# Performance work log

Measured on AMD Instinct MI355X. Metric: run time of the kernel, lower is better.

## Reference

```python
import jax, jax.numpy as jnp
import numpy as np

B, H, S, D = 2, 16, 2048, 64


def setup_inputs() -> dict:
    key = jax.random.key(0)
    kq, kk, kv = jax.random.split(key, 3)
    Q = jax.random.normal(kq, (B, H, S, D), dtype=jnp.float32)
    K = jax.random.normal(kk, (B, H, S, D), dtype=jnp.float32)
    V = jax.random.normal(kv, (B, H, S, D), dtype=jnp.float32)
    # causal mask: True = masked out (matches torch masked_fill_ semantics)
    causal = ~jnp.tril(jnp.ones((S, S), dtype=bool))
    mask = jnp.broadcast_to(causal, (B, H, S, S))
    return {"Q": Q, "K": K, "V": V, "mask": mask}


def reference(Q, K, V, mask):
    d_q = Q.shape[-1]
    scale = 1.0 / np.sqrt(d_q).astype(np.float32)
    # scores: (B, H, S, S)
    scores = jnp.einsum('bhqd,bhkd->bhqk', Q, K) * scale
    scores = jnp.where(mask, jnp.float32(-1e9), scores)
    attention = jax.nn.softmax(scores, axis=-1)
    context = jnp.einsum('bhqk,bhkd->bhqd', attention, V)
    return (context, attention)
```

## Files before the change

kernel.cpp:

```cpp
#include <hip/hip_runtime.h>
#include <hip/hip_bf16.h>


constexpr int SEQ = 2048;
constexpr int HD  = 64;
constexpr int NHEADS = 32;
constexpr int QT  = 64;
constexpr int NT  = SEQ / QT;

typedef __bf16 bf16x8 __attribute__((ext_vector_type(8)));
typedef unsigned short u16x8 __attribute__((ext_vector_type(8)));
typedef unsigned short u16x4 __attribute__((ext_vector_type(4)));
typedef float f32x4 __attribute__((ext_vector_type(4)));
typedef unsigned short us;

__device__ __forceinline__ us f2bf(float x) {
  unsigned u = __builtin_bit_cast(unsigned, x);
  return (us)((u + 0x7fffu + ((u >> 16) & 1u)) >> 16);
}
__device__ __forceinline__ float bf2f(us b) {
  return __builtin_bit_cast(float, (unsigned)b << 16);
}

#define GLOAD_LDS(gp, lp)                                                        \
  __builtin_amdgcn_global_load_lds(                                             \
      (const __attribute__((address_space(1))) void*)(gp),                      \
      (__attribute__((address_space(3))) void*)(lp), 16, 0, 0)

__device__ __forceinline__ void stage8k(const us* img, us* lds, int w, int l) {
  const char* g = (const char*)img + w * 2048 + l * 16;
  char* s = (char*)lds + w * 2048;
  GLOAD_LDS(g, s);
  GLOAD_LDS(g + 1024, s + 1024);
}

__global__ void prep_kernel(const float* __restrict__ Qg,
                            const float* __restrict__ Kg,
                            const float* __restrict__ Vg,
                            us* __restrict__ ws) {
  const int tile = blockIdx.x & (NT - 1);
  const int bh   = blockIdx.x >> 5;
  const int t = threadIdx.x;
  const size_t tOff = ((size_t)bh * SEQ + (size_t)tile * QT) * HD;
  us* Qi = ws + ((size_t)bh * NT + tile) * 4096;
  us* Ki = Qi + (size_t)NHEADS * NT * 4096;
  us* Vi = Ki + (size_t)NHEADS * NT * 4096;

  #pragma unroll
  for (int g0 = 0; g0 < 2; ++g0) {
    const int g = t + 256 * g0;
    const int r = g >> 3, c8 = g & 7;
    const int cp = (8 * c8) ^ ((r & 7) << 3);
    const float* qs = Qg + tOff + (size_t)r * HD + cp;
    const float* ks = Kg + tOff + (size_t)r * HD + cp;
    u16x8 q, k;
    #pragma unroll
    for (int j = 0; j < 8; ++j) { q[j] = f2bf(qs[j]); k[j] = f2bf(ks[j]); }
    *(u16x8*)(Qi + 8 * g) = q;
    *(u16x8*)(Ki + 8 * g) = k;
  }
  #pragma unroll
  for (int g0 = 0; g0 < 2; ++g0) {
    const int g = t + 256 * g0;
    const int d = g >> 3, k8 = g & 7;
    const int kp = (8 * k8) ^ ((d & 7) << 3);
    const float* vs = Vg + tOff + d;
    u16x8 v;
    #pragma unroll
    for (int j = 0; j < 8; ++j) v[j] = f2bf(vs[(size_t)(kp + j) * HD]);
    *(u16x8*)(Vi + 8 * g) = v;
  }
}

__launch_bounds__(256, 3)
__global__ void attn_main(const us* __restrict__ ws, float* __restrict__ out) {
  const int fb = blockIdx.x;
  const int bh = fb & (NHEADS - 1);
  const int pi = fb >> 5;
  const int t  = threadIdx.x;
  const int l  = t & 63;
  const int w  = t >> 6;
  const int l16 = l & 15;
  const int lg  = l >> 4;

  __shared__ __align__(16) us Qs[4096];
  __shared__ __align__(16) us Ks[2][4096];
  __shared__ __align__(16) us Vs[2][4096];
  __shared__ __align__(16) us Ps[4][1024];

  const us* Qi = ws + (size_t)bh * NT * 4096;
  const us* Ki = Qi + (size_t)NHEADS * NT * 4096;
  const us* Vi = Ki + (size_t)NHEADS * NT * 4096;

  float* ctx = out + (size_t)bh * SEQ * HD;
  float* att = out + (size_t)NHEADS * SEQ * HD + (size_t)bh * SEQ * SEQ;

  const float KC = 0.18033688011112042f;

  for (int half = 0; half < 2; ++half) {
    const int qt = half ? (NT - 1 - pi) : pi;
    const int qbase = qt * QT;
    const int qg = qbase + w * 16 + l16;

    stage8k(Qi + (size_t)qt * 4096, Qs, w, l);
    stage8k(Ki, Ks[0], w, l);
    {
      const int zc0 = (qt + 1) * QT;
      const int nz4 = (SEQ - zc0) >> 2;
      for (int r = 0; r < QT; ++r) {
        float* rowp = att + (size_t)(qbase + r) * SEQ + zc0;
        for (int c = t; c < nz4; c += 256)
          __builtin_nontemporal_store((f32x4){0.f, 0.f, 0.f, 0.f}, (f32x4*)(rowp + 4 * c));
      }
    }
    __syncthreads();

    bf16x8 aq[2];
    #pragma unroll
    for (int ks = 0; ks < 2; ++ks) {
      const int qr = w * 16 + l16;
      const int d0 = ks * 32 + lg * 8;
      const int idx = (qr * 64 + d0) ^ ((qr & 7) << 3);
      aq[ks] = __builtin_bit_cast(bf16x8, *(const u16x8*)(&Qs[idx]));
    }

    float rsum = 0.f;
    {
      int cur = 0;
      for (int kt = 0; kt <= qt; ++kt) {
        if (kt < qt) stage8k(Ki + (size_t)(kt + 1) * 4096, Ks[cur ^ 1], w, l);
        const us* krb = Ks[cur];
        const int kb = kt * QT;
        #pragma unroll
        for (int ct = 0; ct < 4; ++ct) {
          f32x4 acc = {0.f, 0.f, 0.f, 0.f};
          #pragma unroll
          for (int ks = 0; ks < 2; ++ks) {
            const int kr = ct * 16 + l16;
            const int d0 = ks * 32 + lg * 8;
            const int idx = (kr * 64 + d0) ^ ((kr & 7) << 3);
            bf16x8 bk = __builtin_bit_cast(bf16x8, *(const u16x8*)(&krb[idx]));
            acc = __builtin_amdgcn_mfma_f32_16x16x32_bf16(bk, aq[ks], acc, 0, 0, 0);
          }
          const int kg0 = kb + ct * 16 + lg * 4;
          #pragma unroll
          for (int r = 0; r < 4; ++r) {
            float e = __builtin_amdgcn_exp2f(acc[r] * KC);
            rsum += (kg0 + r <= qg) ? e : 0.f;
          }
        }
        __syncthreads();
        cur ^= 1;
      }
    }
    stage8k(Ki, Ks[0], w, l);
    stage8k(Vi, Vs[0], w, l);
    rsum += __shfl_xor(rsum, 16);
    rsum += __shfl_xor(rsum, 32);
    const float inv = 1.f / rsum;
    __syncthreads();

    f32x4 oacc[4];
    #pragma unroll
    for (int ct = 0; ct < 4; ++ct) oacc[ct] = (f32x4){0.f, 0.f, 0.f, 0.f};

    {
      int cur = 0;
      for (int kt = 0; kt <= qt; ++kt) {
        if (kt < qt) {
          stage8k(Ki + (size_t)(kt + 1) * 4096, Ks[cur ^ 1], w, l);
          stage8k(Vi + (size_t)(kt + 1) * 4096, Vs[cur ^ 1], w, l);
        }
        const us* krb = Ks[cur];
        const us* vrb = Vs[cur];
        const int kb = kt * QT;

        #pragma unroll
        for (int ct = 0; ct < 4; ++ct) {
          f32x4 acc = {0.f, 0.f, 0.f, 0.f};
          #pragma unroll
          for (int ks = 0; ks < 2; ++ks) {
            const int kr = ct * 16 + l16;
            const int d0 = ks * 32 + lg * 8;
            const int idx = (kr * 64 + d0) ^ ((kr & 7) << 3);
            bf16x8 bk = __builtin_bit_cast(bf16x8, *(const u16x8*)(&krb[idx]));
            acc = __builtin_amdgcn_mfma_f32_16x16x32_bf16(bk, aq[ks], acc, 0, 0, 0);
          }
          const int kg0 = kb + ct * 16 + lg * 4;
          u16x4 pb;
          #pragma unroll
          for (int r = 0; r < 4; ++r) {
            float e = __builtin_amdgcn_exp2f(acc[r] * KC) * inv;
            pb[r] = f2bf((kg0 + r <= qg) ? e : 0.f);
          }
          const int pidx = (l16 * 64 + ct * 16 + lg * 4) ^ ((l16 & 7) << 3);
          *(u16x4*)(&Ps[w][pidx]) = pb;
        }

        #pragma unroll
        for (int j = 0; j < 4; ++j) {
          const int rloc = lg + 4 * j;
          const int idx = (rloc * 64 + 4 * l16) ^ ((rloc & 7) << 3);
          u16x4 p4 = *(const u16x4*)(&Ps[w][idx]);
          f32x4 pv = { bf2f(p4[0]), bf2f(p4[1]), bf2f(p4[2]), bf2f(p4[3]) };
          __builtin_nontemporal_store(pv,
              (f32x4*)(att + (size_t)(qbase + w * 16 + rloc) * SEQ + kb + 4 * l16));
        }

        bf16x8 pa[2];
        #pragma unroll
        for (int ks = 0; ks < 2; ++ks) {
          const int pidx = (l16 * 64 + ks * 32 + lg * 8) ^ ((l16 & 7) << 3);
          pa[ks] = __builtin_bit_cast(bf16x8, *(const u16x8*)(&Ps[w][pidx]));
        }
        #pragma unroll
        for (int ct = 0; ct < 4; ++ct) {
          #pragma unroll
          for (int ks = 0; ks < 2; ++ks) {
            const int dr = ct * 16 + l16;
            const int key0 = ks * 32 + lg * 8;
            const int vidx = (dr * 64 + key0) ^ ((dr & 7) << 3);
            bf16x8 av = __builtin_bit_cast(bf16x8, *(const u16x8*)(&vrb[vidx]));
            oacc[ct] = __builtin_amdgcn_mfma_f32_16x16x32_bf16(av, pa[ks], oacc[ct], 0, 0, 0);
          }
        }

        __syncthreads();
        cur ^= 1;
      }
    }

    #pragma unroll
    for (int ct = 0; ct < 4; ++ct)
      __builtin_nontemporal_store(oacc[ct],
          (f32x4*)(ctx + (size_t)qg * HD + ct * 16 + lg * 4));
  }
}

__launch_bounds__(256, 2)
__global__ void attn_fallback(const float* __restrict__ Qg,
                              const float* __restrict__ Kg,
                              const float* __restrict__ Vg,
                              float* __restrict__ out) {
  const int fb = blockIdx.x;
  const int bh = fb & (NHEADS - 1);
  const int pi = fb >> 5;
  const int t  = threadIdx.x;
  const int l  = t & 63;
  const int w  = t >> 6;
  const int l16 = l & 15;
  const int lg  = l >> 4;

  __shared__ __align__(16) us Qs[QT * HD];
  __shared__ __align__(16) us Ks[QT * HD];
  __shared__ __align__(16) us Vs[QT * HD];
  __shared__ __align__(16) us Ps[4][16 * QT];

  const size_t hoff = (size_t)bh * SEQ * HD;
  const float* Qh = Qg + hoff;
  const float* Kh = Kg + hoff;
  const float* Vh = Vg + hoff;
  float* ctx = out + hoff;
  float* att = out + (size_t)NHEADS * SEQ * HD + (size_t)bh * SEQ * SEQ;

  auto load_tile = [&](const float* src, f32x4 (&reg)[4]) {
    #pragma unroll
    for (int j = 0; j < 4; ++j) {
      const int f = t + 256 * j;
      reg[j] = *(const f32x4*)(src + (size_t)(f >> 4) * HD + 4 * (f & 15));
    }
  };
  auto write_k = [&](const f32x4 (&reg)[4], us* dst) {
    #pragma unroll
    for (int j = 0; j < 4; ++j) {
      const int f = t + 256 * j;
      const int r = f >> 4, c4 = f & 15;
      const int idx = (r * 64 + 4 * c4) ^ ((r & 7) << 3);
      u16x4 b = { f2bf(reg[j].x), f2bf(reg[j].y), f2bf(reg[j].z), f2bf(reg[j].w) };
      *(u16x4*)(&dst[idx]) = b;
    }
  };
  auto write_vv = [&](const f32x4 (&reg)[4], us* dst) {
    #pragma unroll
    for (int j = 0; j < 4; ++j) {
      const int f = t + 256 * j;
      const int r = f >> 4, c4 = f & 15;
      const int idx = (r * 64 + 4 * c4) ^ (((r >> 3) & 3) << 4);
      u16x4 b = { f2bf(reg[j].x), f2bf(reg[j].y), f2bf(reg[j].z), f2bf(reg[j].w) };
      *(u16x4*)(&dst[idx]) = b;
    }
  };

  const float sc = 0.125f;

  for (int half = 0; half < 2; ++half) {
    const int qt = half ? (NT - 1 - pi) : pi;
    const int qbase = qt * QT;
    const int qg = qbase + w * 16 + l16;

    __syncthreads();
    {
      const int zc0 = (qt + 1) * QT;
      const int nz4 = (SEQ - zc0) >> 2;
      for (int r = 0; r < QT; ++r) {
        float* rowp = att + (size_t)(qbase + r) * SEQ + zc0;
        for (int c = t; c < nz4; c += 256)
          __builtin_nontemporal_store((f32x4){0.f, 0.f, 0.f, 0.f}, (f32x4*)(rowp + 4 * c));
      }
    }
    {
      f32x4 qreg[4];
      load_tile(Qh + (size_t)qbase * HD, qreg);
      write_k(qreg, Qs);
    }
    __syncthreads();

    bf16x8 aq[2];
    #pragma unroll
    for (int ks = 0; ks < 2; ++ks) {
      const int qr = w * 16 + l16;
      const int d0 = ks * 32 + lg * 8;
      const int idx = (qr * 64 + d0) ^ ((qr & 7) << 3);
      aq[ks] = __builtin_bit_cast(bf16x8, *(const u16x8*)(&Qs[idx]));
    }

    float rsum = 0.f;
    {
      f32x4 kreg[4];
      load_tile(Kh, kreg);
      write_k(kreg, Ks);
      __syncthreads();
      for (int kt = 0; kt <= qt; ++kt) {
        if (kt < qt) load_tile(Kh + (size_t)(kt + 1) * QT * HD, kreg);
        const int kb = kt * QT;
        #pragma unroll
        for (int ct = 0; ct < 4; ++ct) {
          f32x4 acc = {0.f, 0.f, 0.f, 0.f};
          #pragma unroll
          for (int ks = 0; ks < 2; ++ks) {
            const int kr = ct * 16 + l16;
            const int d0 = ks * 32 + lg * 8;
            const int idx = (kr * 64 + d0) ^ ((kr & 7) << 3);
            bf16x8 bk = __builtin_bit_cast(bf16x8, *(const u16x8*)(&Ks[idx]));
            acc = __builtin_amdgcn_mfma_f32_16x16x32_bf16(bk, aq[ks], acc, 0, 0, 0);
          }
          const int kg0 = kb + ct * 16 + lg * 4;
          #pragma unroll
          for (int r = 0; r < 4; ++r) {
            float e = __expf(acc[r] * sc);
            rsum += (kg0 + r <= qg) ? e : 0.f;
          }
        }
        __syncthreads();
        if (kt < qt) write_k(kreg, Ks);
        __syncthreads();
      }
    }
    rsum += __shfl_xor(rsum, 16);
    rsum += __shfl_xor(rsum, 32);
    const float inv = 1.f / rsum;

    f32x4 oacc[4];
    #pragma unroll
    for (int ct = 0; ct < 4; ++ct) oacc[ct] = (f32x4){0.f, 0.f, 0.f, 0.f};

    {
      f32x4 kreg[4], vreg[4];
      load_tile(Kh, kreg);
      load_tile(Vh, vreg);
      write_k(kreg, Ks);
      write_vv(vreg, Vs);
      __syncthreads();
      for (int kt = 0; kt <= qt; ++kt) {
        if (kt < qt) {
          load_tile(Kh + (size_t)(kt + 1) * QT * HD, kreg);
          load_tile(Vh + (size_t)(kt + 1) * QT * HD, vreg);
        }
        const int kb = kt * QT;
        #pragma unroll
        for (int ct = 0; ct < 4; ++ct) {
          f32x4 acc = {0.f, 0.f, 0.f, 0.f};
          #pragma unroll
          for (int ks = 0; ks < 2; ++ks) {
            const int kr = ct * 16 + l16;
            const int d0 = ks * 32 + lg * 8;
            const int idx = (kr * 64 + d0) ^ ((kr & 7) << 3);
            bf16x8 bk = __builtin_bit_cast(bf16x8, *(const u16x8*)(&Ks[idx]));
            acc = __builtin_amdgcn_mfma_f32_16x16x32_bf16(bk, aq[ks], acc, 0, 0, 0);
          }
          const int kg0 = kb + ct * 16 + lg * 4;
          u16x4 pb;
          #pragma unroll
          for (int r = 0; r < 4; ++r) {
            float e = __expf(acc[r] * sc) * inv;
            pb[r] = f2bf((kg0 + r <= qg) ? e : 0.f);
          }
          const int pidx = (l16 * 64 + ct * 16 + lg * 4) ^ ((l16 & 7) << 3);
          *(u16x4*)(&Ps[w][pidx]) = pb;
        }
        #pragma unroll
        for (int ct = 0; ct < 4; ++ct) {
          #pragma unroll
          for (int ks = 0; ks < 2; ++ks) {
            const int key0 = ks * 32 + lg * 8;
            const int pidx = (l16 * 64 + key0) ^ ((l16 & 7) << 3);
            bf16x8 pa = __builtin_bit_cast(bf16x8, *(const u16x8*)(&Ps[w][pidx]));
            bf16x8 av;
            const int dcol = ct * 16 + l16;
            const int xorv = ((key0 >> 3) & 3) << 4;
            #pragma unroll
            for (int j = 0; j < 8; ++j)
              av[j] = __builtin_bit_cast(__bf16, Vs[((key0 + j) * 64 + dcol) ^ xorv]);
            oacc[ct] = __builtin_amdgcn_mfma_f32_16x16x32_bf16(av, pa, oacc[ct], 0, 0, 0);
          }
        }
        __syncthreads();
        #pragma unroll
        for (int j = 0; j < 4; ++j) {
          const int f = t + 256 * j;
          const int r = f >> 4, c4 = f & 15;
          const int ww = r >> 4, qr = r & 15;
          const int idx = (qr * 64 + 4 * c4) ^ ((qr & 7) << 3);
          u16x4 pb = *(const u16x4*)(&Ps[ww][idx]);
          f32x4 pv = { bf2f(pb[0]), bf2f(pb[1]), bf2f(pb[2]), bf2f(pb[3]) };
          __builtin_nontemporal_store(pv,
              (f32x4*)(att + (size_t)(qbase + r) * SEQ + kb + 4 * c4));
        }
        if (kt < qt) {
          write_k(kreg, Ks);
          write_vv(vreg, Vs);
        }
        __syncthreads();
      }
    }
    #pragma unroll
    for (int ct = 0; ct < 4; ++ct)
      *(f32x4*)(ctx + (size_t)qg * HD + ct * 16 + lg * 4) = oacc[ct];
  }
}

extern "C" void kernel_launch(void* const* d_in, const int* in_sizes, int n_in,
                              void* d_out, int out_size, void* d_ws, size_t ws_size,
                              hipStream_t stream) {
  const float* Q = (const float*)d_in[0];
  const float* K = (const float*)d_in[1];
  const float* V = (const float*)d_in[2];
  float* out = (float*)d_out;
  const size_t NEED = (size_t)3 * NHEADS * NT * 4096 * sizeof(us);
  if (ws_size >= NEED && d_ws != nullptr) {
    us* wsp = (us*)d_ws;
    prep_kernel<<<dim3(NHEADS * NT), dim3(256), 0, stream>>>(Q, K, V, wsp);
    attn_main<<<dim3(NT / 2 * NHEADS), dim3(256), 0, stream>>>(wsp, out);
  } else {
    attn_fallback<<<dim3(NT / 2 * NHEADS), dim3(256), 0, stream>>>(Q, K, V, out);
  }
}
```

Before: 142.1 us.

## Split paired query tiles into separate blocks and tighten pipeline sync

Each block of attn_main previously handled two query tiles, one early and one late, to balance the causal work. Now each block handles a single query tile, launched longest-first, so the grid doubles to 1024 blocks. The Q tile is loaded straight from global into registers, which frees the Qs shared buffer, and the occupancy hint rises from 3 to 4 blocks per CU. The second-pass loop replaces __syncthreads with a manual s_waitcnt vmcnt(4) plus s_barrier and sched barriers, so the next K/V prefetch can stay in flight across the barrier. The trade-offs are more blocks to schedule, the pairing-based balance now resting on launch order, and hand-written waitcnt counts that must match the number of outstanding global-to-LDS loads.

New measurement: 169.0 us. 19.0% more time.

```diff
diff --git a/kernel.cpp b/kernel.cpp
--- a/kernel.cpp
+++ b/kernel.cpp
@@ -72,18 +72,20 @@
   }
 }
 
-__launch_bounds__(256, 3)
+__launch_bounds__(256, 4)
 __global__ void attn_main(const us* __restrict__ ws, float* __restrict__ out) {
   const int fb = blockIdx.x;
-  const int bh = fb & (NHEADS - 1);
-  const int pi = fb >> 5;
+  const int g8 = fb >> 8;
+  const int r  = fb & 255;
+  const int bh = r & (NHEADS - 1);
+  const int p  = (r >> 5) | ((g8 & 1) << 3);
+  const int qt = (g8 >> 1) ? p : (NT - 1 - p);
   const int t  = threadIdx.x;
   const int l  = t & 63;
   const int w  = t >> 6;
   const int l16 = l & 15;
   const int lg  = l >> 4;
 
-  __shared__ __align__(16) us Qs[4096];
   __shared__ __align__(16) us Ks[2][4096];
   __shared__ __align__(16) us Vs[2][4096];
   __shared__ __align__(16) us Ps[4][1024];
@@ -96,145 +98,145 @@
   float* att = out + (size_t)NHEADS * SEQ * HD + (size_t)bh * SEQ * SEQ;
 
   const float KC = 0.18033688011112042f;
-
-  for (int half = 0; half < 2; ++half) {
-    const int qt = half ? (NT - 1 - pi) : pi;
-    const int qbase = qt * QT;
-    const int qg = qbase + w * 16 + l16;
-
-    stage8k(Qi + (size_t)qt * 4096, Qs, w, l);
-    stage8k(Ki, Ks[0], w, l);
-    {
-      const int zc0 = (qt + 1) * QT;
-      const int nz4 = (SEQ - zc0) >> 2;
-      for (int r = 0; r < QT; ++r) {
-        float* rowp = att + (size_t)(qbase + r) * SEQ + zc0;
-        for (int c = t; c < nz4; c += 256)
-          __builtin_nontemporal_store((f32x4){0.f, 0.f, 0.f, 0.f}, (f32x4*)(rowp + 4 * c));
-      }
-    }
-    __syncthreads();
-
-    bf16x8 aq[2];
+  const int qbase = qt * QT;
+  const int qg = qbase + w * 16 + l16;
+
+  bf16x8 aq[2];
+  {
+    const int qr = w * 16 + l16;
     #pragma unroll
     for (int ks = 0; ks < 2; ++ks) {
-      const int qr = w * 16 + l16;
-      const int d0 = ks * 32 + lg * 8;
-      const int idx = (qr * 64 + d0) ^ ((qr & 7) << 3);
-      aq[ks] = __builtin_bit_cast(bf16x8, *(const u16x8*)(&Qs[idx]));
-    }
-
-    float rsum = 0.f;
-    {
-      int cur = 0;
-      for (int kt = 0; kt <= qt; ++kt) {
-        if (kt < qt) stage8k(Ki + (size_t)(kt + 1) * 4096, Ks[cur ^ 1], w, l);
-        const us* krb = Ks[cur];
-        const int kb = kt * QT;
-        #pragma unroll
-        for (int ct = 0; ct < 4; ++ct) {
-          f32x4 acc = {0.f, 0.f, 0.f, 0.f};
-          #pragma unroll
-          for (int ks = 0; ks < 2; ++ks) {
-            const int kr = ct * 16 + l16;
-            const int d0 = ks * 32 + lg * 8;
-            const int idx = (kr * 64 + d0) ^ ((kr & 7) << 3);
-            bf16x8 bk = __builtin_bit_cast(bf16x8, *(const u16x8*)(&krb[idx]));
-            acc = __builtin_amdgcn_mfma_f32_16x16x32_bf16(bk, aq[ks], acc, 0, 0, 0);
-          }
-          const int kg0 = kb + ct * 16 + lg * 4;
-          #pragma unroll
-          for (int r = 0; r < 4; ++r) {
-            float e = __builtin_amdgcn_exp2f(acc[r] * KC);
-            rsum += (kg0 + r <= qg) ? e : 0.f;
-          }
-        }
-        __syncthreads();
-        cur ^= 1;
-      }
-    }
-    stage8k(Ki, Ks[0], w, l);
-    stage8k(Vi, Vs[0], w, l);
-    rsum += __shfl_xor(rsum, 16);
-    rsum += __shfl_xor(rsum, 32);
-    const float inv = 1.f / rsum;
-    __syncthreads();
-
-    f32x4 oacc[4];
-    #pragma unroll
-    for (int ct = 0; ct < 4; ++ct) oacc[ct] = (f32x4){0.f, 0.f, 0.f, 0.f};
-
-    {
-      int cur = 0;
-      for (int kt = 0; kt <= qt; ++kt) {
-        if (kt < qt) {
-          stage8k(Ki + (size_t)(kt + 1) * 4096, Ks[cur ^ 1], w, l);
-          stage8k(Vi + (size_t)(kt + 1) * 4096, Vs[cur ^ 1], w, l);
-        }
-        const us* krb = Ks[cur];
-        const us* vrb = Vs[cur];
-        const int kb = kt * QT;
-
-        #pragma unroll
-        for (int ct = 0; ct < 4; ++ct) {
-          f32x4 acc = {0.f, 0.f, 0.f, 0.f};
-          #pragma unroll
-          for (int ks = 0; ks < 2; ++ks) {
-            const int kr = ct * 16 + l16;
-            const int d0 = ks * 32 + lg * 8;
-            const int idx = (kr * 64 + d0) ^ ((kr & 7) << 3);
-            bf16x8 bk = __builtin_bit_cast(bf16x8, *(const u16x8*)(&krb[idx]));
-            acc = __builtin_amdgcn_mfma_f32_16x16x32_bf16(bk, aq[ks], acc, 0, 0, 0);
-          }
-          const int kg0 = kb + ct * 16 + lg * 4;
-          u16x4 pb;
-          #pragma unroll
-          for (int r = 0; r < 4; ++r) {
-            float e = __builtin_amdgcn_exp2f(acc[r] * KC) * inv;
-            pb[r] = f2bf((kg0 + r <= qg) ? e : 0.f);
-          }
-          const int pidx = (l16 * 64 + ct * 16 + lg * 4) ^ ((l16 & 7) << 3);
-          *(u16x4*)(&Ps[w][pidx]) = pb;
-        }
-
-        #pragma unroll
-        for (int j = 0; j < 4; ++j) {
-          const int rloc = lg + 4 * j;
-          const int idx = (rloc * 64 + 4 * l16) ^ ((rloc & 7) << 3);
-          u16x4 p4 = *(const u16x4*)(&Ps[w][idx]);
-          f32x4 pv = { bf2f(p4[0]), bf2f(p4[1]), bf2f(p4[2]), bf2f(p4[3]) };
-          __builtin_nontemporal_store(pv,
-              (f32x4*)(att + (size_t)(qbase + w * 16 + rloc) * SEQ + kb + 4 * l16));
-        }
-
-        bf16x8 pa[2];
+      const int idx = (qr * 64 + ks * 32 + lg * 8) ^ ((qr & 7) << 3);
+      aq[ks] = __builtin_bit_cast(bf16x8, *(const u16x8*)(&Qi[(size_t)qt * 4096 + idx]));
+    }
+  }
+
+  stage8k(Ki, Ks[0], w, l);
+  {
+    const int zc0 = (qt + 1) * QT;
+    const int nz4 = (SEQ - zc0) >> 2;
+    for (int rr = 0; rr < QT; ++rr) {
+      float* rowp = att + (size_t)(qbase + rr) * SEQ + zc0;
+      for (int c = t; c < nz4; c += 256)
+        __builtin_nontemporal_store((f32x4){0.f, 0.f, 0.f, 0.f}, (f32x4*)(rowp + 4 * c));
+    }
+  }
+  __syncthreads();
+
+  float rsum = 0.f;
+  {
+    int cur = 0;
+    for (int kt = 0; kt <= qt; ++kt) {
+      if (kt < qt) stage8k(Ki + (size_t)(kt + 1) * 4096, Ks[cur ^ 1], w, l);
+      const us* krb = Ks[cur];
+      const int kb = kt * QT;
+      #pragma unroll
+      for (int ct = 0; ct < 4; ++ct) {
+        f32x4 acc = {0.f, 0.f, 0.f, 0.f};
         #pragma unroll
         for (int ks = 0; ks < 2; ++ks) {
-          const int pidx = (l16 * 64 + ks * 32 + lg * 8) ^ ((l16 & 7) << 3);
-          pa[ks] = __builtin_bit_cast(bf16x8, *(const u16x8*)(&Ps[w][pidx]));
-        }
-        #pragma unroll
-        for (int ct = 0; ct < 4; ++ct) {
-          #pragma unroll
-          for (int ks = 0; ks < 2; ++ks) {
-            const int dr = ct * 16 + l16;
-            const int key0 = ks * 32 + lg * 8;
-            const int vidx = (dr * 64 + key0) ^ ((dr & 7) << 3);
-            bf16x8 av = __builtin_bit_cast(bf16x8, *(const u16x8*)(&vrb[vidx]));
-            oacc[ct] = __builtin_amdgcn_mfma_f32_16x16x32_bf16(av, pa[ks], oacc[ct], 0, 0, 0);
-          }
-        }
-
-        __syncthreads();
-        cur ^= 1;
-      }
-    }
-
-    #pragma unroll
-    for (int ct = 0; ct < 4; ++ct)
-      __builtin_nontemporal_store(oacc[ct],
-          (f32x4*)(ctx + (size_t)qg * HD + ct * 16 + lg * 4));
-  }
+          const int kr = ct * 16 + l16;
+          const int idx = (kr * 64 + ks * 32 + lg * 8) ^ ((kr & 7) << 3);
+          bf16x8 bk = __builtin_bit_cast(bf16x8, *(const u16x8*)(&krb[idx]));
+          acc = __builtin_amdgcn_mfma_f32_16x16x32_bf16(bk, aq[ks], acc, 0, 0, 0);
+        }
+        const int kg0 = kb + ct * 16 + lg * 4;
+        #pragma unroll
+        for (int rr = 0; rr < 4; ++rr) {
+          float e = __builtin_amdgcn_exp2f(acc[rr] * KC);
+          rsum += (kg0 + rr <= qg) ? e : 0.f;
+        }
+      }
+      __syncthreads();
+      cur ^= 1;
+    }
+  }
+  stage8k(Ki, Ks[0], w, l);
+  stage8k(Vi, Vs[0], w, l);
+  rsum += __shfl_xor(rsum, 16);
+  rsum += __shfl_xor(rsum, 32);
+  const float inv = 1.f / rsum;
+  __syncthreads();
+
+  f32x4 oacc[4];
+  #pragma unroll
+  for (int ct = 0; ct < 4; ++ct) oacc[ct] = (f32x4){0.f, 0.f, 0.f, 0.f};
+
+  {
+    int cur = 0;
+    for (int kt = 0; kt <= qt; ++kt) {
+      if (kt < qt) {
+        stage8k(Ki + (size_t)(kt + 1) * 4096, Ks[cur ^ 1], w, l);
+        stage8k(Vi + (size_t)(kt + 1) * 4096, Vs[cur ^ 1], w, l);
+      }
+      __builtin_amdgcn_sched_barrier(0);
+      const us* krb = Ks[cur];
+      const us* vrb = Vs[cur];
+      const int kb = kt * QT;
+
+      #pragma unroll
+      for (int ct = 0; ct < 4; ++ct) {
+        f32x4 acc = {0.f, 0.f, 0.f, 0.f};
+        #pragma unroll
+        for (int ks = 0; ks < 2; ++ks) {
+          const int kr = ct * 16 + l16;
+          const int idx = (kr * 64 + ks * 32 + lg * 8) ^ ((kr & 7) << 3);
+          bf16x8 bk = __builtin_bit_cast(bf16x8, *(const u16x8*)(&krb[idx]));
+          acc = __builtin_amdgcn_mfma_f32_16x16x32_bf16(bk, aq[ks], acc, 0, 0, 0);
+        }
+        const int kg0 = kb + ct * 16 + lg * 4;
+        u16x4 pb;
+        #pragma unroll
+        for (int rr = 0; rr < 4; ++rr) {
+          float e = __builtin_amdgcn_exp2f(acc[rr] * KC) * inv;
+          pb[rr] = f2bf((kg0 + rr <= qg) ? e : 0.f);
+        }
+        const int pidx = (l16 * 64 + ct * 16 + lg * 4) ^ ((l16 & 7) << 3);
+        *(u16x4*)(&Ps[w][pidx]) = pb;
+      }
+
+      #pragma unroll
+      for (int j = 0; j < 4; ++j) {
+        const int rloc = lg + 4 * j;
+        const int idx = (rloc * 64 + 4 * l16) ^ ((rloc & 7) << 3);
+        u16x4 p4 = *(const u16x4*)(&Ps[w][idx]);
+        f32x4 pv = { bf2f(p4[0]), bf2f(p4[1]), bf2f(p4[2]), bf2f(p4[3]) };
+        __builtin_nontemporal_store(pv,
+            (f32x4*)(att + (size_t)(qbase + w * 16 + rloc) * SEQ + kb + 4 * l16));
+      }
+
+      bf16x8 pa[2];
+      #pragma unroll
+      for (int ks = 0; ks < 2; ++ks) {
+        const int pidx = (l16 * 64 + ks * 32 + lg * 8) ^ ((l16 & 7) << 3);
+        pa[ks] = __builtin_bit_cast(bf16x8, *(const u16x8*)(&Ps[w][pidx]));
+      }
+      #pragma unroll
+      for (int ct = 0; ct < 4; ++ct) {
+        #pragma unroll
+        for (int ks = 0; ks < 2; ++ks) {
+          const int dr = ct * 16 + l16;
+          const int vidx = (dr * 64 + ks * 32 + lg * 8) ^ ((dr & 7) << 3);
+          bf16x8 av = __builtin_bit_cast(bf16x8, *(const u16x8*)(&vrb[vidx]));
+          oacc[ct] = __builtin_amdgcn_mfma_f32_16x16x32_bf16(av, pa[ks], oacc[ct], 0, 0, 0);
+        }
+      }
+
+      if (kt < qt) {
+        asm volatile("s_waitcnt vmcnt(4) lgkmcnt(0)" ::: "memory");
+      } else {
+        asm volatile("s_waitcnt lgkmcnt(0)" ::: "memory");
+      }
+      __builtin_amdgcn_s_barrier();
+      __builtin_amdgcn_sched_barrier(0);
+      cur ^= 1;
+    }
+  }
+
+  #pragma unroll
+  for (int ct = 0; ct < 4; ++ct)
+    __builtin_nontemporal_store(oacc[ct],
+        (f32x4*)(ctx + (size_t)qg * HD + ct * 16 + lg * 4));
 }
 
 __launch_bounds__(256, 2)
@@ -274,8 +276,8 @@
     #pragma unroll
     for (int j = 0; j < 4; ++j) {
       const int f = t + 256 * j;
-      const int r = f >> 4, c4 = f & 15;
-      const int idx = (r * 64 + 4 * c4) ^ ((r & 7) << 3);
+      const int rr = f >> 4, c4 = f & 15;
+      const int idx = (rr * 64 + 4 * c4) ^ ((rr & 7) << 3);
       u16x4 b = { f2bf(reg[j].x), f2bf(reg[j].y), f2bf(reg[j].z), f2bf(reg[j].w) };
       *(u16x4*)(&dst[idx]) = b;
     }
@@ -284,8 +286,8 @@
     #pragma unroll
     for (int j = 0; j < 4; ++j) {
       const int f = t + 256 * j;
-      const int r = f >> 4, c4 = f & 15;
-      const int idx = (r * 64 + 4 * c4) ^ (((r >> 3) & 3) << 4);
+      const int rr = f >> 4, c4 = f & 15;
+      const int idx = (rr * 64 + 4 * c4) ^ (((rr >> 3) & 3) << 4);
       u16x4 b = { f2bf(reg[j].x), f2bf(reg[j].y), f2bf(reg[j].z), f2bf(reg[j].w) };
       *(u16x4*)(&dst[idx]) = b;
     }
@@ -302,8 +304,8 @@
     {
       const int zc0 = (qt + 1) * QT;
       const int nz4 = (SEQ - zc0) >> 2;
-      for (int r = 0; r < QT; ++r) {
-        float* rowp = att + (size_t)(qbase + r) * SEQ + zc0;
+      for (int rr = 0; rr < QT; ++rr) {
+        float* rowp = att + (size_t)(qbase + rr) * SEQ + zc0;
         for (int c = t; c < nz4; c += 256)
           __builtin_nontemporal_store((f32x4){0.f, 0.f, 0.f, 0.f}, (f32x4*)(rowp + 4 * c));
       }
@@ -319,8 +321,7 @@
     #pragma unroll
     for (int ks = 0; ks < 2; ++ks) {
       const int qr = w * 16 + l16;
-      const int d0 = ks * 32 + lg * 8;
-      const int idx = (qr * 64 + d0) ^ ((qr & 7) << 3);
+      const int idx = (qr * 64 + ks * 32 + lg * 8) ^ ((qr & 7) << 3);
       aq[ks] = __builtin_bit_cast(bf16x8, *(const u16x8*)(&Qs[idx]));
     }
 
@@ -339,16 +340,15 @@
           #pragma unroll
           for (int ks = 0; ks < 2; ++ks) {
             const int kr = ct * 16 + l16;
-            const int d0 = ks * 32 + lg * 8;
-            const int idx = (kr * 64 + d0) ^ ((kr & 7) << 3);
+            const int idx = (kr * 64 + ks * 32 + lg * 8) ^ ((kr & 7) << 3);
             bf16x8 bk = __builtin_bit_cast(bf16x8, *(const u16x8*)(&Ks[idx]));
             acc = __builtin_amdgcn_mfma_f32_16x16x32_bf16(bk, aq[ks], acc, 0, 0, 0);
           }
           const int kg0 = kb + ct * 16 + lg * 4;
           #pragma unroll
-          for (int r = 0; r < 4; ++r) {
-            float e = __expf(acc[r] * sc);
-            rsum += (kg0 + r <= qg) ? e : 0.f;
+          for (int rr = 0; rr < 4; ++rr) {
+            float e = __expf(acc[rr] * sc);
+            rsum += (kg0 + rr <= qg) ? e : 0.f;
           }
         }
         __syncthreads();
@@ -383,17 +383,16 @@
           #pragma unroll
           for (int ks = 0; ks < 2; ++ks) {
             const int kr = ct * 16 + l16;
-            const int d0 = ks * 32 + lg * 8;
-            const int idx = (kr * 64 + d0) ^ ((kr & 7) << 3);
+            const int idx = (kr * 64 + ks * 32 + lg * 8) ^ ((kr & 7) << 3);
             bf16x8 bk = __builtin_bit_cast(bf16x8, *(const u16x8*)(&Ks[idx]));
             acc = __builtin_amdgcn_mfma_f32_16x16x32_bf16(bk, aq[ks], acc, 0, 0, 0);
           }
           const int kg0 = kb + ct * 16 + lg * 4;
           u16x4 pb;
           #pragma unroll
-          for (int r = 0; r < 4; ++r) {
-            float e = __expf(acc[r] * sc) * inv;
-            pb[r] = f2bf((kg0 + r <= qg) ? e : 0.f);
+          for (int rr = 0; rr < 4; ++rr) {
+            float e = __expf(acc[rr] * sc) * inv;
+            pb[rr] = f2bf((kg0 + rr <= qg) ? e : 0.f);
           }
           const int pidx = (l16 * 64 + ct * 16 + lg * 4) ^ ((l16 & 7) << 3);
           *(u16x4*)(&Ps[w][pidx]) = pb;
@@ -418,13 +417,13 @@
         #pragma unroll
         for (int j = 0; j < 4; ++j) {
           const int f = t + 256 * j;
-          const int r = f >> 4, c4 = f & 15;
-          const int ww = r >> 4, qr = r & 15;
+          const int rr = f >> 4, c4 = f & 15;
+          const int ww = rr >> 4, qr = rr & 15;
           const int idx = (qr * 64 + 4 * c4) ^ ((qr & 7) << 3);
           u16x4 pb = *(const u16x4*)(&Ps[ww][idx]);
           f32x4 pv = { bf2f(pb[0]), bf2f(pb[1]), bf2f(pb[2]), bf2f(pb[3]) };
           __builtin_nontemporal_store(pv,
-              (f32x4*)(att + (size_t)(qbase + r) * SEQ + kb + 4 * c4));
+              (f32x4*)(att + (size_t)(qbase + rr) * SEQ + kb + 4 * c4));
         }
         if (kt < qt) {
           write_k(kreg, Ks);
@@ -450,7 +449,7 @@
   if (ws_size >= NEED && d_ws != nullptr) {
     us* wsp = (us*)d_ws;
     prep_kernel<<<dim3(NHEADS * NT), dim3(256), 0, stream>>>(Q, K, V, wsp);
-    attn_main<<<dim3(NT / 2 * NHEADS), dim3(256), 0, stream>>>(wsp, out);
+    attn_main<<<dim3(NT * NHEADS), dim3(256), 0, stream>>>(wsp, out);
   } else {
     attn_fallback<<<dim3(NT / 2 * NHEADS), dim3(256), 0, stream>>>(Q, K, V, out);
   }
```
